# Optimization experiments

Measured on AMD Instinct MI355X. Metric: run time of the kernel, lower is better.

The kernel has to match this reference:

```python
import jax, jax.numpy as jnp
import numpy as np

H = 16            # num heads
D = 64            # head dim
HID = 1024        # hidden size
ALPHA = 1.0       # < 2 -> power-law kernel
BANDWIDTH = 1.0
A = 0.5           # doubly-stochastic exponent
RADIUS = 1.0      # sphere radius
EPS = 1e-7


def setup_inputs() -> dict:
    key = jax.random.key(0)
    ks = jax.random.split(key, 5)
    x = jax.random.normal(ks[0], (2, 2048, HID), dtype=jnp.float32)
    s = 1.0 / np.sqrt(HID)
    qkv_w = jax.random.normal(ks[1], (3 * HID, HID), dtype=jnp.float32) * s
    qkv_b = jnp.zeros((3 * HID,), dtype=jnp.float32)
    out_w = jax.random.normal(ks[2], (HID, HID), dtype=jnp.float32) * s
    out_b = jnp.zeros((HID,), dtype=jnp.float32)
    return {"x": x, "qkv_w": qkv_w, "qkv_b": qkv_b, "out_w": out_w, "out_b": out_b}


def _l2norm(t):
    # torch F.normalize(p=2, dim=-1): divide by max(||t||, 1e-12)
    n = jnp.sqrt(jnp.sum(t * t, axis=-1, keepdims=True))
    return t / jnp.maximum(n, 1e-12)


def reference(x, qkv_w, qkv_b, out_w, out_b):
    B, S, _ = x.shape
    qkv = x @ qkv_w.T + qkv_b                       # [B,S,3*HID]
    q, k, v = jnp.split(qkv, 3, axis=-1)
    # [B,H,S,D]
    q = _l2norm(q.reshape(B, S, H, D).transpose(0, 2, 1, 3))
    k = _l2norm(k.reshape(B, S, H, D).transpose(0, 2, 1, 3))
    v = v.reshape(B, S, H, D).transpose(0, 2, 1, 3)
    # geodesic distance on the sphere
    cos = jnp.clip(jnp.einsum('bhsd,bhtd->bhst', q, k), -1.0 + EPS, 1.0 - EPS)
    g_dist = jnp.arccos(cos) * RADIUS               # [B,H,S,S]
    # alpha < 2: power-law kernel
    attn_score = (1.0 + g_dist / jnp.sqrt(BANDWIDTH)) ** (-(D + ALPHA))
    # doubly-stochastic-style rescale: diag(row^-a) @ K @ diag(col^-a)
    row = attn_score.sum(-1) ** (-A)                # [B,H,S]
    col = attn_score.sum(-2) ** (-A)                # [B,H,S]
    k_tilde = row[..., :, None] * attn_score * col[..., None, :]
    # F.normalize(p=1, dim=3): divide by max(sum |.|, 1e-12); entries >= 0
    probs = k_tilde / jnp.maximum(k_tilde.sum(-1, keepdims=True), 1e-12)
    out = jnp.einsum('bhst,bhtd->bhsd', probs, v)   # [B,H,S,D]
    out = out.transpose(0, 2, 1, 3).reshape(B, S, HID)
    return out @ out_w.T + out_b
```

## Files before the change

kernel.cpp:

```cpp
#include <hip/hip_runtime.h>
#include <math.h>

#define NH   16
#define HD   64
#define HIDN 1024
#define NB   2
#define SEQ  2048
#define ROWS (NB*SEQ)
#define BH   (NB*NH)

typedef __attribute__((ext_vector_type(8))) short bf16x8;
typedef __attribute__((ext_vector_type(8))) _Float16 f16x8;
typedef __attribute__((ext_vector_type(4))) float f32x4;
typedef __attribute__((ext_vector_type(2))) float f32x2;
typedef _Float16 f16;

typedef const __attribute__((address_space(1))) void GV;
typedef __attribute__((address_space(3))) void LV;
__device__ __forceinline__ void glds16(const void* g, void* l) {
    __builtin_amdgcn_global_load_lds((GV*)g, (LV*)l, 16, 0, 0);
}

__device__ __forceinline__ unsigned short f2bf(float f) {
    unsigned u = __float_as_uint(f);
    u += 0x7FFF + ((u >> 16) & 1);
    return (unsigned short)(u >> 16);
}
__device__ __forceinline__ bf16x8 ldfrag(const unsigned short* p) {
    return *(const bf16x8*)p;
}
__device__ __forceinline__ f16x8 ldfragh(const f16* p) {
    return *(const f16x8*)p;
}
__device__ __forceinline__ f32x4 mfma16(bf16x8 a, bf16x8 b, f32x4 c) {
    return __builtin_amdgcn_mfma_f32_16x16x32_bf16(a, b, c, 0, 0, 0);
}
__device__ __forceinline__ f32x4 mfma16h(f16x8 a, f16x8 b, f32x4 c) {
    return __builtin_amdgcn_mfma_f32_16x16x32_f16(a, b, c, 0, 0, 0);
}

__device__ __forceinline__ f32x2 log2_1pacos_pair(float c0, float c1) {
    f32x2 u = { fmaxf(1.0f - c0, 0.0f), fmaxf(1.0f - c1, 0.0f) };
    f32x2 s = { __builtin_amdgcn_sqrtf(u.x), __builtin_amdgcn_sqrtf(u.y) };
    f32x2 p = u * 2.68532e-3f + 7.89259e-3f;
    p = u * p + 2.6516504e-2f;
    p = u * p + 1.1785113e-1f;
    p = u * p + 1.4142136f;
    f32x2 t = s * p + 1.0f;
    return (f32x2){ __builtin_amdgcn_logf(t.x), __builtin_amdgcn_logf(t.y) };
}
__device__ __forceinline__ unsigned packbf(f32x2 w) {
    return (__float_as_uint(w.x) >> 16) | (__float_as_uint(w.y) & 0xffff0000u);
}

__global__ __launch_bounds__(256)
void conv_f16(const float* __restrict__ src, f16* __restrict__ dst) {
    int i = (blockIdx.x * 256 + threadIdx.x) * 8;
    float4 a = *(const float4*)(src + i);
    float4 b = *(const float4*)(src + i + 4);
    f16x8 o = { (f16)a.x, (f16)a.y, (f16)a.z, (f16)a.w,
                (f16)b.x, (f16)b.y, (f16)b.z, (f16)b.w };
    *(f16x8*)(dst + i) = o;
}

__global__ __launch_bounds__(256)
void gemm_nt_f16(const f16* __restrict__ A, const f16* __restrict__ B,
                 const float* __restrict__ bias, float* __restrict__ C,
                 int M, int N, int K)
{
    __shared__ f16 As[128 * 32];
    __shared__ f16 Bs[128 * 32];
    const int tid = threadIdx.x;
    const int lane = tid & 63, w = tid >> 6;
    const int ln = lane & 15, lq = lane >> 4;
    const int wm = (w >> 1) * 64, wn = (w & 1) * 64;
    const int m0 = blockIdx.x * 128, n0 = blockIdx.y * 128;

    const int grow = lane >> 2;
    const int gcol = (lane & 3) * 8;
    const f16* Ab = A + (size_t)(m0 + w * 32 + grow) * K + gcol;
    const f16* Bb = B + (size_t)(n0 + w * 32 + grow) * K + gcol;
    f16* Asw = As + (w * 32) * 32;
    f16* Bsw = Bs + (w * 32) * 32;

    f32x4 acc[4][4];
    #pragma unroll
    for (int i = 0; i < 4; ++i)
        #pragma unroll
        for (int j = 0; j < 4; ++j) acc[i][j] = (f32x4){0.f, 0.f, 0.f, 0.f};

    for (int kc = 0; kc < K; kc += 32) {
        __syncthreads();
        #pragma unroll
        for (int i = 0; i < 2; ++i) {
            glds16(Ab + (size_t)(i * 16) * K + kc, Asw + (i * 16) * 32);
            glds16(Bb + (size_t)(i * 16) * K + kc, Bsw + (i * 16) * 32);
        }
        __syncthreads();
        f16x8 af[4], bf[4];
        #pragma unroll
        for (int i = 0; i < 4; ++i)
            af[i] = *(const f16x8*)&As[(wm + i * 16 + ln) * 32 + lq * 8];
        #pragma unroll
        for (int j = 0; j < 4; ++j)
            bf[j] = *(const f16x8*)&Bs[(wn + j * 16 + ln) * 32 + lq * 8];
        #pragma unroll
        for (int i = 0; i < 4; ++i)
            #pragma unroll
            for (int j = 0; j < 4; ++j)
                acc[i][j] = mfma16h(af[i], bf[j], acc[i][j]);
    }

    #pragma unroll
    for (int i = 0; i < 4; ++i) {
        #pragma unroll
        for (int j = 0; j < 4; ++j) {
            int colIdx = n0 + wn + j * 16 + ln;
            float bs = bias[colIdx];
            #pragma unroll
            for (int r = 0; r < 4; ++r) {
                int row = m0 + wm + i * 16 + lq * 4 + r;
                C[(size_t)row * N + colIdx] = acc[i][j][r] + bs;
            }
        }
    }
}

__global__ __launch_bounds__(256)
void normalize_qk_f16(const float* __restrict__ qkv,
                      f16* __restrict__ qf, f16* __restrict__ kf)
{
    int w    = blockIdx.x * 4 + (threadIdx.x >> 6);
    int lane = threadIdx.x & 63;
    int n = w >> 4, h = w & 15;
    int b = n >> 11, s = n & 2047;
    const float* base = qkv + (size_t)n * 3 * HIDN + h * HD;
    float q = base[lane], k = base[HIDN + lane];
    float qs = q * q, ks = k * k;
    #pragma unroll
    for (int o = 32; o; o >>= 1) { qs += __shfl_xor(qs, o); ks += __shfl_xor(ks, o); }
    q *= 1.0f / fmaxf(sqrtf(qs), 1e-12f);
    k *= 1.0f / fmaxf(sqrtf(ks), 1e-12f);
    size_t idx = ((size_t)((b * NH + h) * SEQ + s)) * HD + lane;
    qf[idx] = (f16)q;
    kf[idx] = (f16)k;
}

__global__ __launch_bounds__(256)
void v_transpose(const float* __restrict__ qkv, unsigned short* __restrict__ vth)
{
    __shared__ float Ls[64][65];
    int bh = blockIdx.y, s0 = blockIdx.x * 64;
    int b = bh >> 4, h = bh & 15;
    int tid = threadIdx.x;
    #pragma unroll
    for (int i = 0; i < 4; ++i) {
        int idx = tid + i * 256;
        int row = idx >> 4, c4 = (idx & 15) * 4;
        float4 v = *(const float4*)&qkv[((size_t)(b * SEQ + s0 + row)) * 3 * HIDN
                                        + 2 * HIDN + h * HD + c4];
        Ls[row][c4+0] = v.x; Ls[row][c4+1] = v.y; Ls[row][c4+2] = v.z; Ls[row][c4+3] = v.w;
    }
    __syncthreads();
    int d = tid >> 2, sb = (tid & 3) * 16;
    unsigned short hi[16];
    #pragma unroll
    for (int j = 0; j < 16; ++j) hi[j] = f2bf(Ls[sb + j][d]);
    size_t o = ((size_t)bh * HD + d) * SEQ + s0 + sb;
    *(uint4*)&vth[o]     = *(uint4*)&hi[0];
    *(uint4*)&vth[o + 8] = *(uint4*)&hi[8];
}

#define KSTR 72

__global__ __launch_bounds__(256)
void col_sum_f16(const f16* __restrict__ qf, const f16* __restrict__ kf,
                 float* __restrict__ colp)
{
    __shared__ __align__(16) f16 Qs[64 * KSTR];
    int bh = blockIdx.y;
    int tid = threadIdx.x, w = tid >> 6, lane = tid & 63, ln = lane & 15, lq = lane >> 4;
    int m0 = blockIdx.x * 64 + w * 16;
    const int sb0 = blockIdx.z * (SEQ / 128);
    const f16* qb = qf + (size_t)bh * SEQ * HD;
    const int sr = tid >> 3;
    const int sc = (tid & 7) * 8;

    size_t rowK = ((size_t)bh * SEQ + m0 + ln) * HD;
    f16x8 kf0 = ldfragh(kf + rowK + lq * 8), kf1 = ldfragh(kf + rowK + 32 + lq * 8);

    uint4 qa = *(const uint4*)(qb + (size_t)(sb0 * 64 + sr) * HD + sc);
    uint4 qc = *(const uint4*)(qb + (size_t)(sb0 * 64 + sr + 32) * HD + sc);

    f32x2 cacc01 = {0.f, 0.f}, cacc23 = {0.f, 0.f};
    #pragma unroll 1
    for (int st = sb0; st < sb0 + SEQ / 128; ++st) {
        __syncthreads();
        *(uint4*)&Qs[sr * KSTR + sc] = qa;
        *(uint4*)&Qs[(sr + 32) * KSTR + sc] = qc;
        int sn = (st + 1 < sb0 + SEQ / 128) ? (st + 1) * 64 : sb0 * 64;
        qa = *(const uint4*)(qb + (size_t)(sn + sr) * HD + sc);
        qc = *(const uint4*)(qb + (size_t)(sn + sr + 32) * HD + sc);
        __syncthreads();
        #pragma unroll
        for (int nt = 0; nt < 4; ++nt) {
            const f16* qp = &Qs[(nt * 16 + ln) * KSTR + lq * 8];
            f32x4 sacc = {0.f, 0.f, 0.f, 0.f};
            sacc = mfma16h(kf0, *(const f16x8*)qp, sacc);
            sacc = mfma16h(kf1, *(const f16x8*)(qp + 32), sacc);
            f32x2 l01 = log2_1pacos_pair(sacc[0], sacc[1]) * -65.0f;
            f32x2 l23 = log2_1pacos_pair(sacc[2], sacc[3]) * -65.0f;
            cacc01 += (f32x2){ __builtin_amdgcn_exp2f(l01.x),
                               __builtin_amdgcn_exp2f(l01.y) };
            cacc23 += (f32x2){ __builtin_amdgcn_exp2f(l23.x),
                               __builtin_amdgcn_exp2f(l23.y) };
        }
    }
    float cacc[4] = {cacc01.x, cacc01.y, cacc23.x, cacc23.y};
    #pragma unroll
    for (int r = 0; r < 4; ++r) {
        float v = cacc[r];
        v += __shfl_xor(v, 1); v += __shfl_xor(v, 2);
        v += __shfl_xor(v, 4); v += __shfl_xor(v, 8);
        if (ln == 0)
            colp[(size_t)blockIdx.z * BH * SEQ + (size_t)bh * SEQ + m0 + lq * 4 + r] = v;
    }
}

__global__ __launch_bounds__(256)
void col_finalize(const float* __restrict__ colp, float* __restrict__ col)
{
    int i = (blockIdx.x * 256 + threadIdx.x) * 4;
    float4 a = *(const float4*)&colp[i];
    float4 b = *(const float4*)&colp[(size_t)BH * SEQ + i];
    float4 o;
    o.x = -0.5f * __builtin_amdgcn_logf(a.x + b.x);
    o.y = -0.5f * __builtin_amdgcn_logf(a.y + b.y);
    o.z = -0.5f * __builtin_amdgcn_logf(a.z + b.z);
    o.w = -0.5f * __builtin_amdgcn_logf(a.w + b.w);
    *(float4*)&col[i] = o;
}

__global__ __launch_bounds__(256)
void attn_f16(const f16* __restrict__ qf, const f16* __restrict__ kf,
              const unsigned short* __restrict__ vth,
              const float* __restrict__ col,
              float* __restrict__ numb, float* __restrict__ denb)
{
    __shared__ __align__(16) f16 Ks[64 * KSTR];
    __shared__ __align__(16) unsigned short Vs[64 * KSTR];
    __shared__ __align__(16) unsigned short Ws[4][16 * KSTR];
    __shared__ __align__(16) float lcls[64];
    int bh = blockIdx.y;
    int b = bh >> 4, h = bh & 15;
    int tid = threadIdx.x, w = tid >> 6, lane = tid & 63, ln = lane & 15, lq = lane >> 4;
    int m0 = blockIdx.x * 64 + w * 16;
    const int th = blockIdx.z;
    const int tb = th * (SEQ / 128);
    unsigned short* ws = Ws[w];

    const f16* kb = kf + (size_t)bh * SEQ * HD;
    const unsigned short* vb = vth + (size_t)bh * HD * SEQ;
    const float* cb = col + (size_t)bh * SEQ;

    const int sr = tid >> 3;
    const int sc = (tid & 7) * 8;

    size_t rowQ = ((size_t)bh * SEQ + m0 + ln) * HD;
    f16x8 qf0 = ldfragh(qf + rowQ + lq * 8), qf1 = ldfragh(qf + rowQ + 32 + lq * 8);

    bf16x8 ones;
    #pragma unroll
    for (int i = 0; i < 8; ++i) ones[i] = (short)0x3F80;

    f32x4 num[4];
    #pragma unroll
    for (int nt = 0; nt < 4; ++nt) num[nt] = (f32x4){0.f, 0.f, 0.f, 0.f};
    f32x4 den = {0.f, 0.f, 0.f, 0.f};

    uint4 ka = *(const uint4*)(kb + (size_t)(tb * 64 + sr) * HD + sc);
    uint4 kc = *(const uint4*)(kb + (size_t)(tb * 64 + sr + 32) * HD + sc);
    uint4 va = *(const uint4*)(vb + (size_t)sr * SEQ + tb * 64 + sc);
    uint4 vc = *(const uint4*)(vb + (size_t)(sr + 32) * SEQ + tb * 64 + sc);
    float clv = (tid < 64) ? cb[tb * 64 + tid] : 0.f;

    #pragma unroll 1
    for (int tt = tb; tt < tb + SEQ / 128; ++tt) {
        __syncthreads();
        *(uint4*)&Ks[sr * KSTR + sc] = ka;
        *(uint4*)&Ks[(sr + 32) * KSTR + sc] = kc;
        *(uint4*)&Vs[sr * KSTR + sc] = va;
        *(uint4*)&Vs[(sr + 32) * KSTR + sc] = vc;
        if (tid < 64) lcls[tid] = clv;
        int tn = (tt + 1 < tb + SEQ / 128) ? (tt + 1) * 64 : tb * 64;
        ka = *(const uint4*)(kb + (size_t)(tn + sr) * HD + sc);
        kc = *(const uint4*)(kb + (size_t)(tn + sr + 32) * HD + sc);
        va = *(const uint4*)(vb + (size_t)sr * SEQ + tn + sc);
        vc = *(const uint4*)(vb + (size_t)(sr + 32) * SEQ + tn + sc);
        clv = (tid < 64) ? cb[tn + tid] : 0.f;
        __syncthreads();

        #pragma unroll
        for (int nt = 0; nt < 4; ++nt) {
            const f16* kp = &Ks[(nt * 16 + ln) * KSTR + lq * 8];
            f32x4 sacc = {0.f, 0.f, 0.f, 0.f};
            sacc = mfma16h(*(const f16x8*)kp, qf0, sacc);
            sacc = mfma16h(*(const f16x8*)(kp + 32), qf1, sacc);
            float4 cl = *(const float4*)&lcls[nt * 16 + lq * 4];
            f32x2 a01 = log2_1pacos_pair(sacc[0], sacc[1]) * -65.0f
                        + (f32x2){cl.x, cl.y};
            f32x2 a23 = log2_1pacos_pair(sacc[2], sacc[3]) * -65.0f
                        + (f32x2){cl.z, cl.w};
            f32x2 w01 = { __builtin_amdgcn_exp2f(a01.x),
                          __builtin_amdgcn_exp2f(a01.y) };
            f32x2 w23 = { __builtin_amdgcn_exp2f(a23.x),
                          __builtin_amdgcn_exp2f(a23.y) };
            uint2 pw;
            pw.x = packbf(w01);
            pw.y = packbf(w23);
            *(uint2*)(ws + ln * KSTR + nt * 16 + lq * 4) = pw;
        }
        bf16x8 wa0 = ldfrag(ws + ln * KSTR + lq * 8);
        bf16x8 wa1 = ldfrag(ws + ln * KSTR + 32 + lq * 8);
        den = mfma16(wa0, ones, den);
        den = mfma16(wa1, ones, den);
        #pragma unroll
        for (int nt = 0; nt < 4; ++nt) {
            const unsigned short* vp = &Vs[(nt * 16 + ln) * KSTR + lq * 8];
            num[nt] = mfma16(wa0, *(const bf16x8*)vp, num[nt]);
            num[nt] = mfma16(wa1, *(const bf16x8*)(vp + 32), num[nt]);
        }
    }

    const size_t noff = (size_t)th * ROWS * HIDN;
    #pragma unroll
    for (int r = 0; r < 4; ++r) {
        int s = m0 + lq * 4 + r;
        #pragma unroll
        for (int nt = 0; nt < 4; ++nt)
            numb[noff + ((size_t)(b * SEQ + s)) * HIDN + h * HD + nt * 16 + ln] =
                num[nt][r];
        if (ln == 0)
            denb[(size_t)th * BH * SEQ + (size_t)bh * SEQ + s] = den[r];
    }
}

__global__ __launch_bounds__(256)
void finalize_ctx(const float* __restrict__ numb, const float* __restrict__ denb,
                  f16* __restrict__ ctx)
{
    size_t i = ((size_t)blockIdx.x * 256 + threadIdx.x) * 8;
    int row = (int)(i >> 10);
    int cidx = (int)(i & (HIDN - 1));
    int b = row >> 11, s = row & 2047;
    int h = cidx >> 6;
    size_t di = (size_t)(b * NH + h) * SEQ + s;
    float d = denb[di] + denb[(size_t)BH * SEQ + di];
    float inv = 1.0f / fmaxf(d, 1e-12f);
    const float* n1 = numb + (size_t)ROWS * HIDN;
    float4 a0 = *(const float4*)&numb[i];
    float4 a1 = *(const float4*)&numb[i + 4];
    float4 b0 = *(const float4*)&n1[i];
    float4 b1 = *(const float4*)&n1[i + 4];
    f16x8 o = { (f16)((a0.x + b0.x) * inv), (f16)((a0.y + b0.y) * inv),
                (f16)((a0.z + b0.z) * inv), (f16)((a0.w + b0.w) * inv),
                (f16)((a1.x + b1.x) * inv), (f16)((a1.y + b1.y) * inv),
                (f16)((a1.z + b1.z) * inv), (f16)((a1.w + b1.w) * inv) };
    *(f16x8*)(ctx + i) = o;
}

extern "C" void kernel_launch(void* const* d_in, const int* in_sizes, int n_in,
                              void* d_out, int out_size, void* d_ws, size_t ws_size,
                              hipStream_t stream) {
    const float* x      = (const float*)d_in[0];
    const float* qkv_w  = (const float*)d_in[1];
    const float* qkv_b  = (const float*)d_in[2];
    const float* out_w  = (const float*)d_in[3];
    const float* out_b  = (const float*)d_in[4];
    float* out = (float*)d_out;

    const size_t NTT = (size_t)BH * SEQ * HD;
    float* qkv = (float*)d_ws;
    float* colp = qkv;
    float* denb = qkv + 2 * (size_t)BH * SEQ;
    float* numb = qkv + 4 * (size_t)BH * SEQ;
    float* col = qkv + (size_t)ROWS * 3 * HIDN;
    f16* xh    = (f16*)(col + (size_t)BH * SEQ);
    f16* wqh   = xh + (size_t)ROWS * HIDN;
    f16* woh   = wqh + (size_t)3 * HIDN * HIDN;
    f16* ctxh  = woh + (size_t)HIDN * HIDN;
    f16* qfp   = ctxh + (size_t)ROWS * HIDN;
    f16* kfp   = qfp + NTT;
    unsigned short* vth = (unsigned short*)(kfp + NTT);

    conv_f16<<<ROWS*HIDN/2048, 256, 0, stream>>>(x, xh);
    conv_f16<<<3*HIDN*HIDN/2048, 256, 0, stream>>>(qkv_w, wqh);
    conv_f16<<<HIDN*HIDN/2048, 256, 0, stream>>>(out_w, woh);

    gemm_nt_f16<<<dim3(ROWS/128, 3*HIDN/128), 256, 0, stream>>>(
        xh, wqh, qkv_b, qkv, ROWS, 3*HIDN, HIDN);
    normalize_qk_f16<<<ROWS*NH/4, 256, 0, stream>>>(qkv, qfp, kfp);
    v_transpose<<<dim3(SEQ/64, BH), 256, 0, stream>>>(qkv, vth);
    col_sum_f16<<<dim3(SEQ/64, BH, 2), 256, 0, stream>>>(qfp, kfp, colp);
    col_finalize<<<BH*SEQ/1024, 256, 0, stream>>>(colp, col);
    attn_f16<<<dim3(SEQ/64, BH, 2), 256, 0, stream>>>(qfp, kfp, vth, col,
                                                      numb, denb);
    finalize_ctx<<<ROWS*HIDN/2048, 256, 0, stream>>>(numb, denb, ctxh);
    gemm_nt_f16<<<dim3(ROWS/128, HIDN/128), 256, 0, stream>>>(
        ctxh, woh, out_b, out, ROWS, HIDN, HIDN);
}
```

Before: 317.8 us.

## Process two 16-row query sub-tiles per wave to reuse K/V tiles

```diff
diff --git a/kernel.cpp b/kernel.cpp
--- a/kernel.cpp
+++ b/kernel.cpp
@@ -241,7 +241,7 @@
     *(float4*)&col[i] = o;
 }
 
-__global__ __launch_bounds__(256)
+__global__ __launch_bounds__(256, 4)
 void attn_f16(const f16* __restrict__ qf, const f16* __restrict__ kf,
               const unsigned short* __restrict__ vth,
               const float* __restrict__ col,
@@ -249,14 +249,14 @@
 {
     __shared__ __align__(16) f16 Ks[64 * KSTR];
     __shared__ __align__(16) unsigned short Vs[64 * KSTR];
-    __shared__ __align__(16) unsigned short Ws[4][16 * KSTR];
+    __shared__ __align__(16) unsigned short Ws[4][32 * KSTR];
     __shared__ __align__(16) float lcls[64];
     int bh = blockIdx.y;
     int b = bh >> 4, h = bh & 15;
     int tid = threadIdx.x, w = tid >> 6, lane = tid & 63, ln = lane & 15, lq = lane >> 4;
-    int m0 = blockIdx.x * 64 + w * 16;
+    int m0 = blockIdx.x * 128 + w * 32;
     const int th = blockIdx.z;
-    const int tb = th * (SEQ / 128);
+    const int tb = th * (SEQ / 2);
     unsigned short* ws = Ws[w];
 
     const f16* kb = kf + (size_t)bh * SEQ * HD;
@@ -266,33 +266,37 @@
     const int sr = tid >> 3;
     const int sc = (tid & 7) * 8;
 
-    size_t rowQ = ((size_t)bh * SEQ + m0 + ln) * HD;
-    f16x8 qf0 = ldfragh(qf + rowQ + lq * 8), qf1 = ldfragh(qf + rowQ + 32 + lq * 8);
+    size_t rowQ0 = ((size_t)bh * SEQ + m0 + ln) * HD;
+    size_t rowQ1 = ((size_t)bh * SEQ + m0 + 16 + ln) * HD;
+    f16x8 qf0 = ldfragh(qf + rowQ0 + lq * 8), qf1 = ldfragh(qf + rowQ0 + 32 + lq * 8);
+    f16x8 qf2 = ldfragh(qf + rowQ1 + lq * 8), qf3 = ldfragh(qf + rowQ1 + 32 + lq * 8);
 
     bf16x8 ones;
     #pragma unroll
     for (int i = 0; i < 8; ++i) ones[i] = (short)0x3F80;
 
-    f32x4 num[4];
-    #pragma unroll
-    for (int nt = 0; nt < 4; ++nt) num[nt] = (f32x4){0.f, 0.f, 0.f, 0.f};
-    f32x4 den = {0.f, 0.f, 0.f, 0.f};
-
-    uint4 ka = *(const uint4*)(kb + (size_t)(tb * 64 + sr) * HD + sc);
-    uint4 kc = *(const uint4*)(kb + (size_t)(tb * 64 + sr + 32) * HD + sc);
-    uint4 va = *(const uint4*)(vb + (size_t)sr * SEQ + tb * 64 + sc);
-    uint4 vc = *(const uint4*)(vb + (size_t)(sr + 32) * SEQ + tb * 64 + sc);
-    float clv = (tid < 64) ? cb[tb * 64 + tid] : 0.f;
+    f32x4 num[2][4];
+    #pragma unroll
+    for (int hs = 0; hs < 2; ++hs)
+        #pragma unroll
+        for (int nt = 0; nt < 4; ++nt) num[hs][nt] = (f32x4){0.f, 0.f, 0.f, 0.f};
+    f32x4 den[2] = { {0.f, 0.f, 0.f, 0.f}, {0.f, 0.f, 0.f, 0.f} };
+
+    uint4 ka = *(const uint4*)(kb + (size_t)(tb + sr) * HD + sc);
+    uint4 kc = *(const uint4*)(kb + (size_t)(tb + sr + 32) * HD + sc);
+    uint4 va = *(const uint4*)(vb + (size_t)sr * SEQ + tb + sc);
+    uint4 vc = *(const uint4*)(vb + (size_t)(sr + 32) * SEQ + tb + sc);
+    float clv = (tid < 64) ? cb[tb + tid] : 0.f;
 
     #pragma unroll 1
-    for (int tt = tb; tt < tb + SEQ / 128; ++tt) {
+    for (int tt = 0; tt < SEQ / 128; ++tt) {
         __syncthreads();
         *(uint4*)&Ks[sr * KSTR + sc] = ka;
         *(uint4*)&Ks[(sr + 32) * KSTR + sc] = kc;
         *(uint4*)&Vs[sr * KSTR + sc] = va;
         *(uint4*)&Vs[(sr + 32) * KSTR + sc] = vc;
         if (tid < 64) lcls[tid] = clv;
-        int tn = (tt + 1 < tb + SEQ / 128) ? (tt + 1) * 64 : tb * 64;
+        int tn = (tt + 1 < SEQ / 128) ? tb + (tt + 1) * 64 : tb;
         ka = *(const uint4*)(kb + (size_t)(tn + sr) * HD + sc);
         kc = *(const uint4*)(kb + (size_t)(tn + sr + 32) * HD + sc);
         va = *(const uint4*)(vb + (size_t)sr * SEQ + tn + sc);
@@ -303,45 +307,62 @@
         #pragma unroll
         for (int nt = 0; nt < 4; ++nt) {
             const f16* kp = &Ks[(nt * 16 + ln) * KSTR + lq * 8];
-            f32x4 sacc = {0.f, 0.f, 0.f, 0.f};
-            sacc = mfma16h(*(const f16x8*)kp, qf0, sacc);
-            sacc = mfma16h(*(const f16x8*)(kp + 32), qf1, sacc);
+            f16x8 kfa = *(const f16x8*)kp, kfc = *(const f16x8*)(kp + 32);
             float4 cl = *(const float4*)&lcls[nt * 16 + lq * 4];
-            f32x2 a01 = log2_1pacos_pair(sacc[0], sacc[1]) * -65.0f
-                        + (f32x2){cl.x, cl.y};
-            f32x2 a23 = log2_1pacos_pair(sacc[2], sacc[3]) * -65.0f
-                        + (f32x2){cl.z, cl.w};
-            f32x2 w01 = { __builtin_amdgcn_exp2f(a01.x),
-                          __builtin_amdgcn_exp2f(a01.y) };
-            f32x2 w23 = { __builtin_amdgcn_exp2f(a23.x),
-                          __builtin_amdgcn_exp2f(a23.y) };
-            uint2 pw;
-            pw.x = packbf(w01);
-            pw.y = packbf(w23);
-            *(uint2*)(ws + ln * KSTR + nt * 16 + lq * 4) = pw;
-        }
-        bf16x8 wa0 = ldfrag(ws + ln * KSTR + lq * 8);
-        bf16x8 wa1 = ldfrag(ws + ln * KSTR + 32 + lq * 8);
-        den = mfma16(wa0, ones, den);
-        den = mfma16(wa1, ones, den);
+            f32x4 s0 = {0.f, 0.f, 0.f, 0.f};
+            s0 = mfma16h(kfa, qf0, s0);
+            s0 = mfma16h(kfc, qf1, s0);
+            f32x4 s1 = {0.f, 0.f, 0.f, 0.f};
+            s1 = mfma16h(kfa, qf2, s1);
+            s1 = mfma16h(kfc, qf3, s1);
+            f32x2 a01 = log2_1pacos_pair(s0[0], s0[1]) * -65.0f + (f32x2){cl.x, cl.y};
+            f32x2 a23 = log2_1pacos_pair(s0[2], s0[3]) * -65.0f + (f32x2){cl.z, cl.w};
+            f32x2 b01 = log2_1pacos_pair(s1[0], s1[1]) * -65.0f + (f32x2){cl.x, cl.y};
+            f32x2 b23 = log2_1pacos_pair(s1[2], s1[3]) * -65.0f + (f32x2){cl.z, cl.w};
+            uint2 pw0, pw1;
+            pw0.x = packbf((f32x2){ __builtin_amdgcn_exp2f(a01.x),
+                                    __builtin_amdgcn_exp2f(a01.y) });
+            pw0.y = packbf((f32x2){ __builtin_amdgcn_exp2f(a23.x),
+                                    __builtin_amdgcn_exp2f(a23.y) });
+            pw1.x = packbf((f32x2){ __builtin_amdgcn_exp2f(b01.x),
+                                    __builtin_amdgcn_exp2f(b01.y) });
+            pw1.y = packbf((f32x2){ __builtin_amdgcn_exp2f(b23.x),
+                                    __builtin_amdgcn_exp2f(b23.y) });
+            *(uint2*)(ws + ln * KSTR + nt * 16 + lq * 4) = pw0;
+            *(uint2*)(ws + (16 + ln) * KSTR + nt * 16 + lq * 4) = pw1;
+        }
+        bf16x8 wa00 = ldfrag(ws + ln * KSTR + lq * 8);
+        bf16x8 wa01 = ldfrag(ws + ln * KSTR + 32 + lq * 8);
+        bf16x8 wa10 = ldfrag(ws + (16 + ln) * KSTR + lq * 8);
+        bf16x8 wa11 = ldfrag(ws + (16 + ln) * KSTR + 32 + lq * 8);
+        den[0] = mfma16(wa00, ones, den[0]);
+        den[0] = mfma16(wa01, ones, den[0]);
+        den[1] = mfma16(wa10, ones, den[1]);
+        den[1] = mfma16(wa11, ones, den[1]);
         #pragma unroll
         for (int nt = 0; nt < 4; ++nt) {
             const unsigned short* vp = &Vs[(nt * 16 + ln) * KSTR + lq * 8];
-            num[nt] = mfma16(wa0, *(const bf16x8*)vp, num[nt]);
-            num[nt] = mfma16(wa1, *(const bf16x8*)(vp + 32), num[nt]);
+            bf16x8 v0 = *(const bf16x8*)vp, v1 = *(const bf16x8*)(vp + 32);
+            num[0][nt] = mfma16(wa00, v0, num[0][nt]);
+            num[0][nt] = mfma16(wa01, v1, num[0][nt]);
+            num[1][nt] = mfma16(wa10, v0, num[1][nt]);
+            num[1][nt] = mfma16(wa11, v1, num[1][nt]);
         }
     }
 
     const size_t noff = (size_t)th * ROWS * HIDN;
     #pragma unroll
-    for (int r = 0; r < 4; ++r) {
-        int s = m0 + lq * 4 + r;
-        #pragma unroll
-        for (int nt = 0; nt < 4; ++nt)
-            numb[noff + ((size_t)(b * SEQ + s)) * HIDN + h * HD + nt * 16 + ln] =
-                num[nt][r];
-        if (ln == 0)
-            denb[(size_t)th * BH * SEQ + (size_t)bh * SEQ + s] = den[r];
+    for (int hs = 0; hs < 2; ++hs) {
+        #pragma unroll
+        for (int r = 0; r < 4; ++r) {
+            int s = m0 + hs * 16 + lq * 4 + r;
+            #pragma unroll
+            for (int nt = 0; nt < 4; ++nt)
+                numb[noff + ((size_t)(b * SEQ + s)) * HIDN + h * HD + nt * 16 + ln] =
+                    num[hs][nt][r];
+            if (ln == 0)
+                denb[(size_t)th * BH * SEQ + (size_t)bh * SEQ + s] = den[hs][r];
+        }
     }
 }
 
@@ -403,8 +424,8 @@
     v_transpose<<<dim3(SEQ/64, BH), 256, 0, stream>>>(qkv, vth);
     col_sum_f16<<<dim3(SEQ/64, BH, 2), 256, 0, stream>>>(qfp, kfp, colp);
     col_finalize<<<BH*SEQ/1024, 256, 0, stream>>>(colp, col);
-    attn_f16<<<dim3(SEQ/64, BH, 2), 256, 0, stream>>>(qfp, kfp, vth, col,
-                                                      numb, denb);
+    attn_f16<<<dim3(SEQ/128, BH, 2), 256, 0, stream>>>(qfp, kfp, vth, col,
+                                                       numb, denb);
     finalize_ctx<<<ROWS*HIDN/2048, 256, 0, stream>>>(numb, denb, ctxh);
     gemm_nt_f16<<<dim3(ROWS/128, HIDN/128), 256, 0, stream>>>(
         ctxh, woh, out_b, out, ROWS, HIDN, HIDN);
```

Result: no change. 318.2 us (+0.1%).
